# Performance work log

Hardware: AMD Instinct MI355X
Metric: run time of the kernel (lower is better)

The kernel has to match this reference:

```python
import jax, jax.numpy as jnp
import numpy as np

E = 8        # num experts
TOP = 2      # top-k
D = 1024     # emb_size


def setup_inputs() -> dict:
    key = jax.random.key(0)
    ks = jax.random.split(key, 8)
    s = 1.0 / np.sqrt(D)
    x = jax.random.normal(ks[0], (4, 2048, D), dtype=jnp.float32)
    Wg = jax.random.uniform(ks[1], (D, E), jnp.float32, -s, s)
    bg = jax.random.uniform(ks[2], (E,), jnp.float32, -s, s)
    W1 = jax.random.uniform(ks[3], (E, D, D), jnp.float32, -s, s)
    b1 = jax.random.uniform(ks[4], (E, D), jnp.float32, -s, s)
    W2 = jax.random.uniform(ks[5], (E, D, D), jnp.float32, -s, s)
    b2 = jax.random.uniform(ks[6], (E, D), jnp.float32, -s, s)
    return {"x": x, "Wg": Wg, "bg": bg, "W1": W1, "b1": b1, "W2": W2, "b2": b2}


def reference(x, Wg, bg, W1, b1, W2, b2):
    x_shape = x.shape
    xt = x.reshape(-1, x_shape[-1])                       # [N, D] tokens
    gate_prob = jax.nn.softmax(xt @ Wg + bg, axis=-1)     # [N, E]
    top_w, top_i = jax.lax.top_k(gate_prob, TOP)          # [N, TOP]
    top_w = jax.nn.softmax(top_w, axis=-1)                # renormalize over top-k
    N = xt.shape[0]
    # combine weights scattered into dense [N, E] (each token has TOP nonzeros)
    comb = jnp.zeros((N, E), xt.dtype).at[jnp.arange(N)[:, None], top_i].add(top_w)
    # per-expert 2-layer MLP applied to all tokens; masked-out tokens get 0 combine weight
    h = jax.nn.relu(jnp.einsum('nd,edf->enf', xt, W1) + b1[:, None, :])   # [E, N, D]
    ye = jnp.einsum('enf,efg->eng', h, W2) + b2[:, None, :]               # [E, N, D]
    y = jnp.einsum('ne,eng->ng', comb, ye)                                # [N, D]
    return y.reshape(x_shape), gate_prob
```

## Files before the change

### kernel.cpp

```cpp
#include <hip/hip_runtime.h>
#include <stdint.h>

#define TOKENS 8192
#define DIM    1024
#define NEXP   8
#define NASSIGN (TOKENS*2)
#define BK     64
#define NKT    (DIM/BK)
#define G1BLK  1088

#define C_ROW   16
#define C_TILE  25
#define C_TOTAL 34

#define WS_CTRL  0
#define WS_TOPE  1024
#define WS_TOPW  (WS_TOPE + NASSIGN*4)
#define WS_PTOK  (WS_TOPW + NASSIGN*4)
#define WS_AROW  (WS_PTOK + NASSIGN*4)
#define WS_XB    (WS_AROW + NASSIGN*4)
#define WS_W1T   (WS_XB  + (size_t)TOKENS*DIM*2)
#define WS_W2T   (WS_W1T + (size_t)NEXP*DIM*DIM*2)
#define WS_H     (WS_W2T + (size_t)NEXP*DIM*DIM*2)
#define WS_YE    WS_XB

#define WGLD (DIM + 4)

typedef __attribute__((ext_vector_type(8))) short short8;
typedef __attribute__((ext_vector_type(4))) float floatx4;

__device__ __forceinline__ uint32_t bfr(float f) {
  uint32_t v = __float_as_uint(f);
  return (v + 0x7FFFu + ((v >> 16) & 1u)) >> 16;
}
__device__ __forceinline__ float b2f(uint32_t u) { return __uint_as_float(u << 16); }

__device__ __forceinline__ void load_lds16(const void* g, void* l) {
  __builtin_amdgcn_global_load_lds(
      (const __attribute__((address_space(1))) uint32_t*)g,
      (__attribute__((address_space(3))) uint32_t*)l, 16, 0, 0);
}

__device__ __forceinline__ void convw_tile(
    const float* __restrict__ src, uint16_t* __restrict__ dst,
    int d0, int f0, uint16_t (*tile)[68], int t) {
  int col = t & 63, rb = (t >> 6) * 16;
  #pragma unroll
  for (int i = 0; i < 16; i++) {
    int dr = rb + i;
    tile[dr][col] = (uint16_t)bfr(src[(size_t)(d0+dr)*DIM + f0 + col]);
  }
  __syncthreads();
  int dg = t & 15, frb = t >> 4;
  #pragma unroll
  for (int i = 0; i < 4; i++) {
    int fr = frb + i * 16;
    uint32_t c0 = tile[dg*4+0][fr], c1 = tile[dg*4+1][fr];
    uint32_t c2 = tile[dg*4+2][fr], c3 = tile[dg*4+3][fr];
    uint2 v;
    v.x = c0 | (c1 << 16);
    v.y = c2 | (c3 << 16);
    *(uint2*)&dst[(size_t)(f0+fr)*DIM + d0 + dg*4] = v;
  }
}

__global__ __launch_bounds__(256) void prep_kernel(
    const float* __restrict__ x, const float* __restrict__ Wg,
    const float* __restrict__ bg, float* __restrict__ gate_out,
    int* __restrict__ top_e, float* __restrict__ top_w,
    uint16_t* __restrict__ xb,
    const float* __restrict__ W1, uint16_t* __restrict__ W1T) {
  __shared__ __align__(16) char smem[NEXP * WGLD * 4];
  int t = threadIdx.x;

  if (blockIdx.x >= 2048) {
    int cb = blockIdx.x - 2048;
    int m  = cb >> 8;
    int d0 = ((cb >> 4) & 15) * 64, f0 = (cb & 15) * 64;
    convw_tile(W1 + (size_t)m*DIM*DIM, W1T + (size_t)m*DIM*DIM,
               d0, f0, (uint16_t (*)[68])smem, t);
    return;
  }

  float* wgs = (float*)smem;
  #pragma unroll
  for (int k = 0; k < 32; k++) {
    int i = k * 256 + t;
    float v = Wg[i];
    wgs[(i & 7) * WGLD + (i >> 3)] = v;
  }
  __syncthreads();

  int wave = t >> 6, lane = t & 63;
  int tok = blockIdx.x * 4 + wave;
  const float4* xr = (const float4*)(x + (size_t)tok * DIM);
  uint2* xw = (uint2*)(xb + (size_t)tok * DIM);

  float4 acc[NEXP];
  #pragma unroll
  for (int e = 0; e < NEXP; e++) acc[e] = make_float4(0.f, 0.f, 0.f, 0.f);

  #pragma unroll
  for (int c = 0; c < 4; c++) {
    float4 xv = xr[c * 64 + lane];
    uint2 o;
    o.x = bfr(xv.x) | (bfr(xv.y) << 16);
    o.y = bfr(xv.z) | (bfr(xv.w) << 16);
    xw[c * 64 + lane] = o;
    int d0 = (c * 64 + lane) * 4;
    #pragma unroll
    for (int e = 0; e < NEXP; e++) {
      float4 wv = *(const float4*)&wgs[e * WGLD + d0];
      acc[e].x = fmaf(xv.x, wv.x, acc[e].x);
      acc[e].y = fmaf(xv.y, wv.y, acc[e].y);
      acc[e].z = fmaf(xv.z, wv.z, acc[e].z);
      acc[e].w = fmaf(xv.w, wv.w, acc[e].w);
    }
  }
  float s[NEXP];
  #pragma unroll
  for (int e = 0; e < NEXP; e++) s[e] = (acc[e].x + acc[e].y) + (acc[e].z + acc[e].w);
  #pragma unroll
  for (int off = 32; off > 0; off >>= 1) {
    #pragma unroll
    for (int e = 0; e < NEXP; e++) s[e] += __shfl_xor(s[e], off);
  }
  if (lane == 0) {
    float lg[NEXP], p[NEXP];
    float mx = -1e30f;
    #pragma unroll
    for (int e = 0; e < NEXP; e++) { lg[e] = s[e] + bg[e]; mx = fmaxf(mx, lg[e]); }
    float sum = 0.f;
    #pragma unroll
    for (int e = 0; e < NEXP; e++) { p[e] = expf(lg[e] - mx); sum += p[e]; }
    float inv = 1.f / sum;
    #pragma unroll
    for (int e = 0; e < NEXP; e++) p[e] *= inv;
    float4* go = (float4*)(gate_out + (size_t)tok * NEXP);
    go[0] = make_float4(p[0], p[1], p[2], p[3]);
    go[1] = make_float4(p[4], p[5], p[6], p[7]);
    int i1 = 0;
    #pragma unroll
    for (int e = 1; e < NEXP; e++) if (p[e] > p[i1]) i1 = e;
    int i2 = (i1 == 0) ? 1 : 0;
    #pragma unroll
    for (int e = 0; e < NEXP; e++) if (e != i1 && p[e] > p[i2]) i2 = e;
    float ev = expf(p[i2] - p[i1]);
    float w1 = 1.f / (1.f + ev), w2 = ev / (1.f + ev);
    top_e[2*tok]   = i1; top_e[2*tok+1] = i2;
    top_w[2*tok]   = w1; top_w[2*tok+1] = w2;
  }
}

__global__ __launch_bounds__(1024) void route_kernel(
    const int* __restrict__ top_e, int* __restrict__ ctrl,
    int* __restrict__ ptok, int* __restrict__ arow) {
  __shared__ int sc[NEXP * 1024];
  __shared__ int scnt[NEXP];
  __shared__ int rowstart[NEXP];
  int t = threadIdx.x;
  int e_loc[16];
  int cnt[NEXP];
  #pragma unroll
  for (int e = 0; e < NEXP; e++) cnt[e] = 0;
  #pragma unroll
  for (int j = 0; j < 16; j++) {
    int e = top_e[t * 16 + j];
    e_loc[j] = e;
    cnt[e]++;
  }
  #pragma unroll
  for (int e = 0; e < NEXP; e++) sc[e * 1024 + t] = cnt[e];
  __syncthreads();
  int wave = t >> 6, lane = t & 63;
  if (wave < NEXP) {
    int running = 0;
    for (int chunk = 0; chunk < 16; chunk++) {
      int idx = wave * 1024 + chunk * 64 + lane;
      int v = sc[idx];
      int incl = v;
      #pragma unroll
      for (int off = 1; off < 64; off <<= 1) {
        int u = __shfl_up(incl, off);
        if (lane >= off) incl += u;
      }
      sc[idx] = running + incl - v;
      running += __shfl(incl, 63);
    }
    if (lane == 0) scnt[wave] = running;
  }
  __syncthreads();
  if (t == 0) {
    int rs = 0, ts = 0;
    for (int e = 0; e < NEXP; e++) {
      ctrl[C_ROW + e] = rs;
      ctrl[C_TILE + e] = ts;
      rowstart[e] = rs;
      int c = scnt[e];
      rs += c;
      ts += (c + 127) >> 7;
    }
    ctrl[C_ROW + NEXP] = rs;
    ctrl[C_TILE + NEXP] = ts;
    ctrl[C_TOTAL] = ts;
  }
  __syncthreads();
  int off[NEXP];
  #pragma unroll
  for (int e = 0; e < NEXP; e++) off[e] = rowstart[e] + sc[e * 1024 + t];
  #pragma unroll
  for (int j = 0; j < 16; j++) {
    int i = t * 16 + j;
    int e = e_loc[j];
    int pos = off[e]++;
    ptok[pos] = i >> 1;
    arow[i] = pos;
  }
}

__device__ __forceinline__ bool sched_map(const int* ctrl, int bid,
                                          int& mtile, int& n0) {
  int total = ctrl[C_TOTAL];
  int spx = (total + 7) >> 3;
  int xcd = bid & 7, j = bid >> 3;
  int slot = j >> 3;
  if (slot >= spx) return false;
  mtile = xcd * spx + slot;
  n0 = (j & 7) * 128;
  return mtile < total;
}

__global__ __launch_bounds__(256, 2) void gemm1_kernel(
    const uint16_t* __restrict__ xb, const uint16_t* __restrict__ w1t,
    const float* __restrict__ b1, const int* __restrict__ ctrl,
    const int* __restrict__ ptok, uint16_t* __restrict__ h,
    const float* __restrict__ W2, uint16_t* __restrict__ w2t) {
  __shared__ __align__(16) uint16_t As[128*BK];
  __shared__ __align__(16) uint16_t Bs[128*BK];
  int t = threadIdx.x;

  if (blockIdx.x >= G1BLK) {
    int cb = blockIdx.x - G1BLK;
    int m  = cb >> 8;
    int d0 = ((cb >> 4) & 15) * 64, f0 = (cb & 15) * 64;
    convw_tile(W2 + (size_t)m*DIM*DIM, w2t + (size_t)m*DIM*DIM,
               d0, f0, (uint16_t (*)[68])As, t);
    return;
  }

  int mtile, n0;
  if (!sched_map(ctrl, blockIdx.x, mtile, n0)) return;
  int e = 0;
  #pragma unroll
  for (int k = 1; k < NEXP; k++) if (mtile >= ctrl[C_TILE + k]) e = k;
  int row0 = ctrl[C_ROW + e] + (mtile - ctrl[C_TILE + e]) * 128;
  int rend = ctrl[C_ROW + e + 1];

  int lane = t & 63, w = t >> 6;
  const uint16_t* gA[4];
  const uint16_t* gB[4];
  #pragma unroll
  for (int i = 0; i < 4; i++) {
    int s = i * 256 + t;
    int row = s >> 3, cs = s & 7;
    int gc = cs ^ (row & 7);
    int ar = row0 + row; if (ar > NASSIGN-1) ar = NASSIGN-1;
    int tok = ptok[ar];
    gA[i] = xb  + (size_t)tok * DIM + gc*8;
    gB[i] = w1t + (size_t)e*DIM*DIM + (size_t)(n0 + row)*DIM + gc*8;
  }
  floatx4 acc[4][4];
  #pragma unroll
  for (int mi = 0; mi < 4; mi++)
    #pragma unroll
    for (int ni = 0; ni < 4; ni++) acc[mi][ni] = (floatx4)(0.f);

  int wm = w & 1, wn = w >> 1;
  int l15 = lane & 15, lq = lane >> 4;

  for (int kt = 0; kt < NKT; kt++) {
    #pragma unroll
    for (int i = 0; i < 4; i++) {
      load_lds16(gA[i], &As[(i*256 + t) * 8]);
      load_lds16(gB[i], &Bs[(i*256 + t) * 8]);
      gA[i] += BK; gB[i] += BK;
    }
    __syncthreads();
    #pragma unroll
    for (int ks = 0; ks < 2; ks++) {
      short8 a[4], b[4];
      #pragma unroll
      for (int mi = 0; mi < 4; mi++) {
        int row = wm*64 + mi*16 + l15;
        int slot = (ks*4 + lq) ^ (row & 7);
        a[mi] = *(const short8*)&As[row*BK + slot*8];
      }
      #pragma unroll
      for (int ni = 0; ni < 4; ni++) {
        int row = wn*64 + ni*16 + l15;
        int slot = (ks*4 + lq) ^ (row & 7);
        b[ni] = *(const short8*)&Bs[row*BK + slot*8];
      }
      #pragma unroll
      for (int mi = 0; mi < 4; mi++)
        #pragma unroll
        for (int ni = 0; ni < 4; ni++)
          acc[mi][ni] = __builtin_amdgcn_mfma_f32_16x16x32_bf16(a[mi], b[ni], acc[mi][ni], 0, 0, 0);
    }
    __syncthreads();
  }
  #pragma unroll
  for (int mi = 0; mi < 4; mi++) {
    #pragma unroll
    for (int r = 0; r < 4; r++) {
      int rt = wm*64 + mi*16 + lq*4 + r;
      int ar = row0 + rt;
      if (ar < rend) {
        #pragma unroll
        for (int ni = 0; ni < 4; ni++) {
          int n = n0 + wn*64 + ni*16 + l15;
          float v = acc[mi][ni][r] + b1[e*DIM + n];
          v = fmaxf(v, 0.f);
          h[(size_t)ar*DIM + n] = (uint16_t)bfr(v);
        }
      }
    }
  }
}

__global__ __launch_bounds__(256, 2) void gemm2_kernel(
    const uint16_t* __restrict__ h, const uint16_t* __restrict__ w2t,
    const float* __restrict__ b2, const int* __restrict__ ctrl,
    uint16_t* __restrict__ yeb) {
  __shared__ __align__(16) uint16_t As[128*BK];
  __shared__ __align__(16) uint16_t Bs[128*BK];
  int mtile, n0;
  if (!sched_map(ctrl, blockIdx.x, mtile, n0)) return;
  int e = 0;
  #pragma unroll
  for (int k = 1; k < NEXP; k++) if (mtile >= ctrl[C_TILE + k]) e = k;
  int row0 = ctrl[C_ROW + e] + (mtile - ctrl[C_TILE + e]) * 128;
  int rend = ctrl[C_ROW + e + 1];

  int t = threadIdx.x, lane = t & 63, w = t >> 6;
  const uint16_t* gA[4];
  const uint16_t* gB[4];
  #pragma unroll
  for (int i = 0; i < 4; i++) {
    int s = i * 256 + t;
    int row = s >> 3, cs = s & 7;
    int gc = cs ^ (row & 7);
    int ar = row0 + row; if (ar > NASSIGN-1) ar = NASSIGN-1;
    gA[i] = h   + (size_t)ar * DIM + gc*8;
    gB[i] = w2t + (size_t)e*DIM*DIM + (size_t)(n0 + row)*DIM + gc*8;
  }
  floatx4 acc[4][4];
  #pragma unroll
  for (int mi = 0; mi < 4; mi++)
    #pragma unroll
    for (int ni = 0; ni < 4; ni++) acc[mi][ni] = (floatx4)(0.f);

  int wm = w & 1, wn = w >> 1;
  int l15 = lane & 15, lq = lane >> 4;

  for (int kt = 0; kt < NKT; kt++) {
    #pragma unroll
    for (int i = 0; i < 4; i++) {
      load_lds16(gA[i], &As[(i*256 + t) * 8]);
      load_lds16(gB[i], &Bs[(i*256 + t) * 8]);
      gA[i] += BK; gB[i] += BK;
    }
    __syncthreads();
    #pragma unroll
    for (int ks = 0; ks < 2; ks++) {
      short8 a[4], b[4];
      #pragma unroll
      for (int mi = 0; mi < 4; mi++) {
        int row = wm*64 + mi*16 + l15;
        int slot = (ks*4 + lq) ^ (row & 7);
        a[mi] = *(const short8*)&As[row*BK + slot*8];
      }
      #pragma unroll
      for (int ni = 0; ni < 4; ni++) {
        int row = wn*64 + ni*16 + l15;
        int slot = (ks*4 + lq) ^ (row & 7);
        b[ni] = *(const short8*)&Bs[row*BK + slot*8];
      }
      #pragma unroll
      for (int mi = 0; mi < 4; mi++)
        #pragma unroll
        for (int ni = 0; ni < 4; ni++)
          acc[mi][ni] = __builtin_amdgcn_mfma_f32_16x16x32_bf16(a[mi], b[ni], acc[mi][ni], 0, 0, 0);
    }
    __syncthreads();
  }
  #pragma unroll
  for (int mi = 0; mi < 4; mi++) {
    #pragma unroll
    for (int r = 0; r < 4; r++) {
      int rt = wm*64 + mi*16 + lq*4 + r;
      int ar = row0 + rt;
      if (ar < rend) {
        #pragma unroll
        for (int ni = 0; ni < 4; ni++) {
          int n = n0 + wn*64 + ni*16 + l15;
          float v = acc[mi][ni][r] + b2[e*DIM + n];
          yeb[(size_t)ar*DIM + n] = (uint16_t)bfr(v);
        }
      }
    }
  }
}

__global__ __launch_bounds__(256) void combine_kernel(
    const uint16_t* __restrict__ yeb, const int* __restrict__ arow,
    const float* __restrict__ top_w, float* __restrict__ y) {
  int t = threadIdx.x;
  int tok = blockIdx.x * 2 + (t >> 7);
  int i = t & 127;
  int r0 = arow[2*tok], r1 = arow[2*tok+1];
  float w0 = top_w[2*tok], w1 = top_w[2*tok+1];
  const uint4* a = (const uint4*)(yeb + (size_t)r0 * DIM);
  const uint4* b = (const uint4*)(yeb + (size_t)r1 * DIM);
  uint4 av = a[i], bv = b[i];
  float4* yo = (float4*)(y + (size_t)tok * DIM + i * 8);
  float4 o0, o1;
  o0.x = w0 * b2f(av.x & 0xFFFFu) + w1 * b2f(bv.x & 0xFFFFu);
  o0.y = w0 * b2f(av.x >> 16)     + w1 * b2f(bv.x >> 16);
  o0.z = w0 * b2f(av.y & 0xFFFFu) + w1 * b2f(bv.y & 0xFFFFu);
  o0.w = w0 * b2f(av.y >> 16)     + w1 * b2f(bv.y >> 16);
  o1.x = w0 * b2f(av.z & 0xFFFFu) + w1 * b2f(bv.z & 0xFFFFu);
  o1.y = w0 * b2f(av.z >> 16)     + w1 * b2f(bv.z >> 16);
  o1.z = w0 * b2f(av.w & 0xFFFFu) + w1 * b2f(bv.w & 0xFFFFu);
  o1.w = w0 * b2f(av.w >> 16)     + w1 * b2f(bv.w >> 16);
  yo[0] = o0;
  yo[1] = o1;
}

extern "C" void kernel_launch(void* const* d_in, const int* in_sizes, int n_in,
                              void* d_out, int out_size, void* d_ws, size_t ws_size,
                              hipStream_t stream) {
  const float* x  = (const float*)d_in[0];
  const float* Wg = (const float*)d_in[1];
  const float* bg = (const float*)d_in[2];
  const float* W1 = (const float*)d_in[3];
  const float* b1 = (const float*)d_in[4];
  const float* W2 = (const float*)d_in[5];
  const float* b2 = (const float*)d_in[6];
  float* out = (float*)d_out;
  char* ws = (char*)d_ws;

  int*      ctrl = (int*)(ws + WS_CTRL);
  int*      tope = (int*)(ws + WS_TOPE);
  float*    topw = (float*)(ws + WS_TOPW);
  int*      ptok = (int*)(ws + WS_PTOK);
  int*      arow = (int*)(ws + WS_AROW);
  uint16_t* xb   = (uint16_t*)(ws + WS_XB);
  uint16_t* w1t  = (uint16_t*)(ws + WS_W1T);
  uint16_t* w2t  = (uint16_t*)(ws + WS_W2T);
  uint16_t* hbuf = (uint16_t*)(ws + WS_H);
  uint16_t* yeb  = (uint16_t*)(ws + WS_YE);

  prep_kernel<<<4096, 256, 0, stream>>>(x, Wg, bg, out + (size_t)TOKENS*DIM,
                                        tope, topw, xb, W1, w1t);
  route_kernel<<<1, 1024, 0, stream>>>(tope, ctrl, ptok, arow);
  gemm1_kernel<<<G1BLK + 2048, 256, 0, stream>>>(xb, w1t, b1, ctrl, ptok, hbuf,
                                                 W2, w2t);
  gemm2_kernel<<<136*8, 256, 0, stream>>>(hbuf, w2t, b2, ctrl, yeb);
  combine_kernel<<<TOKENS/2, 256, 0, stream>>>(yeb, arow, topw, out);
}
```

Before: 266.9 us.

## Fuse routing into gating kernel via last-block atomic counter

Removes the separate single-block route kernel launch by having the last gating block, found through an atomic counter, do the expert histogram, prefix scan and token permutation. A memset clears the counter before each launch. This saves one kernel launch and its gap. The cost is that the routing now runs in one 256-thread block instead of 1024 threads, with 64 serial items per thread, and it reads top_e back from global memory.

```diff
diff --git a/kernel.cpp b/kernel.cpp
--- a/kernel.cpp
+++ b/kernel.cpp
@@ -9,6 +9,7 @@
 #define NKT    (DIM/BK)
 #define G1BLK  1088
 
+#define C_CNT   0
 #define C_ROW   16
 #define C_TILE  25
 #define C_TOTAL 34
@@ -69,8 +70,12 @@
     const float* __restrict__ bg, float* __restrict__ gate_out,
     int* __restrict__ top_e, float* __restrict__ top_w,
     uint16_t* __restrict__ xb,
-    const float* __restrict__ W1, uint16_t* __restrict__ W1T) {
+    const float* __restrict__ W1, uint16_t* __restrict__ W1T,
+    int* __restrict__ ctrl, int* __restrict__ ptok, int* __restrict__ arow) {
   __shared__ __align__(16) char smem[NEXP * WGLD * 4];
+  __shared__ int scnt[NEXP];
+  __shared__ int rowstart[NEXP];
+  __shared__ int is_last;
   int t = threadIdx.x;
 
   if (blockIdx.x >= 2048) {
@@ -82,101 +87,104 @@
     return;
   }
 
-  float* wgs = (float*)smem;
-  #pragma unroll
-  for (int k = 0; k < 32; k++) {
-    int i = k * 256 + t;
-    float v = Wg[i];
-    wgs[(i & 7) * WGLD + (i >> 3)] = v;
-  }
-  __syncthreads();
-
+  {
+    float* wgs = (float*)smem;
+    #pragma unroll
+    for (int k = 0; k < 32; k++) {
+      int i = k * 256 + t;
+      float v = Wg[i];
+      wgs[(i & 7) * WGLD + (i >> 3)] = v;
+    }
+    __syncthreads();
+
+    int wave = t >> 6, lane = t & 63;
+    int tok = blockIdx.x * 4 + wave;
+    const float4* xr = (const float4*)(x + (size_t)tok * DIM);
+    uint2* xw = (uint2*)(xb + (size_t)tok * DIM);
+
+    float4 acc[NEXP];
+    #pragma unroll
+    for (int e = 0; e < NEXP; e++) acc[e] = make_float4(0.f, 0.f, 0.f, 0.f);
+
+    #pragma unroll
+    for (int c = 0; c < 4; c++) {
+      float4 xv = xr[c * 64 + lane];
+      uint2 o;
+      o.x = bfr(xv.x) | (bfr(xv.y) << 16);
+      o.y = bfr(xv.z) | (bfr(xv.w) << 16);
+      xw[c * 64 + lane] = o;
+      int d0 = (c * 64 + lane) * 4;
+      #pragma unroll
+      for (int e = 0; e < NEXP; e++) {
+        float4 wv = *(const float4*)&wgs[e * WGLD + d0];
+        acc[e].x = fmaf(xv.x, wv.x, acc[e].x);
+        acc[e].y = fmaf(xv.y, wv.y, acc[e].y);
+        acc[e].z = fmaf(xv.z, wv.z, acc[e].z);
+        acc[e].w = fmaf(xv.w, wv.w, acc[e].w);
+      }
+    }
+    float s[NEXP];
+    #pragma unroll
+    for (int e = 0; e < NEXP; e++) s[e] = (acc[e].x + acc[e].y) + (acc[e].z + acc[e].w);
+    #pragma unroll
+    for (int off = 32; off > 0; off >>= 1) {
+      #pragma unroll
+      for (int e = 0; e < NEXP; e++) s[e] += __shfl_xor(s[e], off);
+    }
+    if (lane == 0) {
+      float lg[NEXP], p[NEXP];
+      float mx = -1e30f;
+      #pragma unroll
+      for (int e = 0; e < NEXP; e++) { lg[e] = s[e] + bg[e]; mx = fmaxf(mx, lg[e]); }
+      float sum = 0.f;
+      #pragma unroll
+      for (int e = 0; e < NEXP; e++) { p[e] = expf(lg[e] - mx); sum += p[e]; }
+      float inv = 1.f / sum;
+      #pragma unroll
+      for (int e = 0; e < NEXP; e++) p[e] *= inv;
+      float4* go = (float4*)(gate_out + (size_t)tok * NEXP);
+      go[0] = make_float4(p[0], p[1], p[2], p[3]);
+      go[1] = make_float4(p[4], p[5], p[6], p[7]);
+      int i1 = 0;
+      #pragma unroll
+      for (int e = 1; e < NEXP; e++) if (p[e] > p[i1]) i1 = e;
+      int i2 = (i1 == 0) ? 1 : 0;
+      #pragma unroll
+      for (int e = 0; e < NEXP; e++) if (e != i1 && p[e] > p[i2]) i2 = e;
+      float ev = expf(p[i2] - p[i1]);
+      float w1 = 1.f / (1.f + ev), w2 = ev / (1.f + ev);
+      top_e[2*tok]   = i1; top_e[2*tok+1] = i2;
+      top_w[2*tok]   = w1; top_w[2*tok+1] = w2;
+    }
+  }
+
+  __threadfence();
+  __syncthreads();
+  if (t == 0) {
+    int old = __hip_atomic_fetch_add(&ctrl[C_CNT], 1, __ATOMIC_ACQ_REL,
+                                     __HIP_MEMORY_SCOPE_AGENT);
+    is_last = (old == 2047);
+  }
+  __syncthreads();
+  if (!is_last) return;
+  __threadfence();
+
+  int* sc = (int*)smem;
+  int cnt[NEXP];
+  #pragma unroll
+  for (int e = 0; e < NEXP; e++) cnt[e] = 0;
+  for (int j = 0; j < 64; j++) {
+    int e = top_e[t * 64 + j];
+    cnt[e]++;
+  }
+  #pragma unroll
+  for (int e = 0; e < NEXP; e++) sc[e * 256 + t] = cnt[e];
+  __syncthreads();
   int wave = t >> 6, lane = t & 63;
-  int tok = blockIdx.x * 4 + wave;
-  const float4* xr = (const float4*)(x + (size_t)tok * DIM);
-  uint2* xw = (uint2*)(xb + (size_t)tok * DIM);
-
-  float4 acc[NEXP];
-  #pragma unroll
-  for (int e = 0; e < NEXP; e++) acc[e] = make_float4(0.f, 0.f, 0.f, 0.f);
-
-  #pragma unroll
-  for (int c = 0; c < 4; c++) {
-    float4 xv = xr[c * 64 + lane];
-    uint2 o;
-    o.x = bfr(xv.x) | (bfr(xv.y) << 16);
-    o.y = bfr(xv.z) | (bfr(xv.w) << 16);
-    xw[c * 64 + lane] = o;
-    int d0 = (c * 64 + lane) * 4;
-    #pragma unroll
-    for (int e = 0; e < NEXP; e++) {
-      float4 wv = *(const float4*)&wgs[e * WGLD + d0];
-      acc[e].x = fmaf(xv.x, wv.x, acc[e].x);
-      acc[e].y = fmaf(xv.y, wv.y, acc[e].y);
-      acc[e].z = fmaf(xv.z, wv.z, acc[e].z);
-      acc[e].w = fmaf(xv.w, wv.w, acc[e].w);
-    }
-  }
-  float s[NEXP];
-  #pragma unroll
-  for (int e = 0; e < NEXP; e++) s[e] = (acc[e].x + acc[e].y) + (acc[e].z + acc[e].w);
-  #pragma unroll
-  for (int off = 32; off > 0; off >>= 1) {
-    #pragma unroll
-    for (int e = 0; e < NEXP; e++) s[e] += __shfl_xor(s[e], off);
-  }
-  if (lane == 0) {
-    float lg[NEXP], p[NEXP];
-    float mx = -1e30f;
-    #pragma unroll
-    for (int e = 0; e < NEXP; e++) { lg[e] = s[e] + bg[e]; mx = fmaxf(mx, lg[e]); }
-    float sum = 0.f;
-    #pragma unroll
-    for (int e = 0; e < NEXP; e++) { p[e] = expf(lg[e] - mx); sum += p[e]; }
-    float inv = 1.f / sum;
-    #pragma unroll
-    for (int e = 0; e < NEXP; e++) p[e] *= inv;
-    float4* go = (float4*)(gate_out + (size_t)tok * NEXP);
-    go[0] = make_float4(p[0], p[1], p[2], p[3]);
-    go[1] = make_float4(p[4], p[5], p[6], p[7]);
-    int i1 = 0;
-    #pragma unroll
-    for (int e = 1; e < NEXP; e++) if (p[e] > p[i1]) i1 = e;
-    int i2 = (i1 == 0) ? 1 : 0;
-    #pragma unroll
-    for (int e = 0; e < NEXP; e++) if (e != i1 && p[e] > p[i2]) i2 = e;
-    float ev = expf(p[i2] - p[i1]);
-    float w1 = 1.f / (1.f + ev), w2 = ev / (1.f + ev);
-    top_e[2*tok]   = i1; top_e[2*tok+1] = i2;
-    top_w[2*tok]   = w1; top_w[2*tok+1] = w2;
-  }
-}
-
-__global__ __launch_bounds__(1024) void route_kernel(
-    const int* __restrict__ top_e, int* __restrict__ ctrl,
-    int* __restrict__ ptok, int* __restrict__ arow) {
-  __shared__ int sc[NEXP * 1024];
-  __shared__ int scnt[NEXP];
-  __shared__ int rowstart[NEXP];
-  int t = threadIdx.x;
-  int e_loc[16];
-  int cnt[NEXP];
-  #pragma unroll
-  for (int e = 0; e < NEXP; e++) cnt[e] = 0;
-  #pragma unroll
-  for (int j = 0; j < 16; j++) {
-    int e = top_e[t * 16 + j];
-    e_loc[j] = e;
-    cnt[e]++;
-  }
-  #pragma unroll
-  for (int e = 0; e < NEXP; e++) sc[e * 1024 + t] = cnt[e];
-  __syncthreads();
-  int wave = t >> 6, lane = t & 63;
-  if (wave < NEXP) {
+  for (int ee = wave; ee < NEXP; ee += 4) {
     int running = 0;
-    for (int chunk = 0; chunk < 16; chunk++) {
-      int idx = wave * 1024 + chunk * 64 + lane;
+    for (int chunk = 0; chunk < 4; chunk++) {
+      int idx = ee * 256 + chunk * 64 + lane;
       int v = sc[idx];
       int incl = v;
       #pragma unroll
@@ -187,7 +195,7 @@
       sc[idx] = running + incl - v;
       running += __shfl(incl, 63);
     }
-    if (lane == 0) scnt[wave] = running;
+    if (lane == 0) scnt[ee] = running;
   }
   __syncthreads();
   if (t == 0) {
@@ -207,11 +215,10 @@
   __syncthreads();
   int off[NEXP];
   #pragma unroll
-  for (int e = 0; e < NEXP; e++) off[e] = rowstart[e] + sc[e * 1024 + t];
-  #pragma unroll
-  for (int j = 0; j < 16; j++) {
-    int i = t * 16 + j;
-    int e = e_loc[j];
+  for (int e = 0; e < NEXP; e++) off[e] = rowstart[e] + sc[e * 256 + t];
+  for (int j = 0; j < 64; j++) {
+    int i = t * 64 + j;
+    int e = top_e[i];
     int pos = off[e]++;
     ptok[pos] = i >> 1;
     arow[i] = pos;
@@ -461,9 +468,11 @@
   uint16_t* hbuf = (uint16_t*)(ws + WS_H);
   uint16_t* yeb  = (uint16_t*)(ws + WS_YE);
 
+  hipMemsetAsync(ws, 0, 64, stream);
+
   prep_kernel<<<4096, 256, 0, stream>>>(x, Wg, bg, out + (size_t)TOKENS*DIM,
-                                        tope, topw, xb, W1, w1t);
-  route_kernel<<<1, 1024, 0, stream>>>(tope, ctrl, ptok, arow);
+                                        tope, topw, xb, W1, w1t,
+                                        ctrl, ptok, arow);
   gemm1_kernel<<<G1BLK + 2048, 256, 0, stream>>>(xb, w1t, b1, ctrl, ptok, hbuf,
                                                  W2, w2t);
   gemm2_kernel<<<136*8, 256, 0, stream>>>(hbuf, w2t, b2, ctrl, yeb);
```

Result: slower. 467.5 us (+75.2%).
